# Optimization experiments

Measured on AMD Instinct MI355X. Metric: run time of the kernel, lower is better.

## Reference

```python
import jax, jax.numpy as jnp
import numpy as np

EPS = 1e-6
D_MODEL, D_HEAD, COND_F = 1024, 64, 768
N_HEADS = D_MODEL // D_HEAD
BATCH, SEQ = 2, 2048


def _rope_freqs(d_head, n_heads):
    # RoPE.__init__: dim = d_head // 2; count = n_heads * dim // 4 = n_heads * d_head // 8
    d8 = d_head // 8
    log_min, log_max = np.log(np.pi), np.log(10.0 * np.pi)
    f = np.exp(np.linspace(log_min, log_max, n_heads * d8 + 1, dtype=np.float64)[:-1])
    return jnp.asarray(f.reshape(d8, n_heads).T, dtype=jnp.float32)  # [nh, d8]


def _apply_rotary(x, theta):
    # x: [n, nh, l, e], theta: [n, nh, l, d8]; rotate first 2*d8 channels
    d = theta.shape[-1]
    x1, x2, rest = x[..., :d], x[..., d:2 * d], x[..., 2 * d:]
    cos, sin = jnp.cos(theta), jnp.sin(theta)
    y1 = x1 * cos - x2 * sin
    y2 = x2 * cos + x1 * sin
    return jnp.concatenate([y1, y2, rest], axis=-1)


def setup_inputs() -> dict:
    key = jax.random.key(0)
    ks = jax.random.split(key, 6)
    x = jax.random.normal(ks[0], (BATCH, SEQ, D_MODEL), dtype=jnp.float32)
    pos = jnp.broadcast_to(jnp.arange(SEQ, dtype=jnp.float32), (BATCH, SEQ))[..., None]
    cond = jax.random.normal(ks[1], (BATCH, COND_F), dtype=jnp.float32)
    w_norm = jax.random.normal(ks[2], (D_MODEL, COND_F), dtype=jnp.float32) * 0.02
    w_qkv = jax.random.normal(ks[3], (3 * D_MODEL, D_MODEL), dtype=jnp.float32) * 0.02
    scale = jnp.full((N_HEADS,), 10.0, dtype=jnp.float32)
    w_out = jax.random.normal(ks[4], (D_MODEL, D_MODEL), dtype=jnp.float32) * 0.02
    return {"x": x, "pos": pos, "cond": cond, "w_norm": w_norm,
            "w_qkv": w_qkv, "scale": scale, "w_out": w_out}


def reference(x, pos, cond, w_norm, w_qkv, scale, w_out):
    n, l, d = x.shape
    nh, e = N_HEADS, D_HEAD
    skip = x
    # AdaRMSNorm: scale = (linear(cond) + 1) * rsqrt(mean(x^2))
    cond_scale = cond @ w_norm.T + 1.0                      # [n, d]
    mean_sq = jnp.mean(x * x, axis=-1, keepdims=True)       # [n, l, 1]
    xn = x * (cond_scale[:, None, :] * jax.lax.rsqrt(mean_sq + EPS))
    # QKV projection
    qkv = (xn @ w_qkv.T).reshape(n, l, 3, nh, e)
    q = jnp.transpose(qkv[:, :, 0], (0, 2, 1, 3))           # [n, nh, l, e]
    k = jnp.transpose(qkv[:, :, 1], (0, 2, 1, 3))
    v = jnp.transpose(qkv[:, :, 2], (0, 2, 1, 3))
    # cosine-sim scaling
    sqrt_scale = jnp.sqrt(scale)[None, :, None, None]       # [1, nh, 1, 1]
    q = q * (sqrt_scale * jax.lax.rsqrt(jnp.sum(q * q, axis=-1, keepdims=True) + EPS))
    k = k * (sqrt_scale * jax.lax.rsqrt(jnp.sum(k * k, axis=-1, keepdims=True) + EPS))
    # RoPE: theta = pos[..., None] * freqs -> [n, l, nh, d8] -> [n, nh, l, d8]
    freqs = _rope_freqs(e, nh)
    theta = jnp.transpose(pos[..., None] * freqs, (0, 2, 1, 3))
    q = _apply_rotary(q, theta)
    k = _apply_rotary(k, theta)
    # attention with softmax scale = 1.0
    scores = jnp.einsum('nhle,nhme->nhlm', q, k)
    attn = jax.nn.softmax(scores, axis=-1)
    out = jnp.einsum('nhlm,nhme->nhle', attn, v)
    out = jnp.transpose(out, (0, 2, 1, 3)).reshape(n, l, d)
    return out @ w_out.T + skip
```

## Files before the change

kernel.cpp:

```cpp
#include <hip/hip_runtime.h>
#include <math.h>

#define D_MODEL 1024
#define D_HEAD  64
#define N_HEADS 16
#define COND_F  768
#define BATCH   2
#define SEQ     2048
#define NTOK    (BATCH*SEQ)
#define QKV_N   (3*D_MODEL)

typedef unsigned short u16;
typedef __attribute__((ext_vector_type(4))) float  f32x4;
typedef __attribute__((ext_vector_type(8))) __bf16 bfrag;
typedef __attribute__((ext_vector_type(4))) unsigned short u16x4;
typedef __attribute__((ext_vector_type(8))) unsigned short u16x8;

__device__ __forceinline__ u16 f2bf(float f) {
    unsigned u = __builtin_bit_cast(unsigned, f);
    return (u16)((u + 0x7fffu + ((u >> 16) & 1u)) >> 16);
}
__device__ __forceinline__ float bf2f(u16 h) {
    unsigned u = ((unsigned)h) << 16;
    return __builtin_bit_cast(float, u);
}

__device__ __forceinline__ float fexp2(float x) {
    float y;
    asm("v_exp_f32 %0, %1" : "=v"(y) : "v"(x));
    return y;
}

__device__ __forceinline__ void async16(const void* g, void* l) {
    __builtin_amdgcn_global_load_lds(
        (const __attribute__((address_space(1))) unsigned int*)g,
        (__attribute__((address_space(3))) unsigned int*)l, 16, 0, 0);
}

__global__ __launch_bounds__(256) void prep_kernel(const float* __restrict__ wqkv,
                                                   const float* __restrict__ wout,
                                                   u16* __restrict__ wqkv_b,
                                                   u16* __restrict__ wout_b,
                                                   const float* __restrict__ cond,
                                                   const float* __restrict__ w_norm,
                                                   float* __restrict__ cs,
                                                   const float* __restrict__ pos,
                                                   float2* __restrict__ tab) {
    if (blockIdx.x < 2048) {
        int i = blockIdx.x * 256 + threadIdx.x;
        const int n1 = QKV_N * D_MODEL / 8;
        const float* src; u16* dst; int off;
        if (i < n1) { src = wqkv; dst = wqkv_b; off = i * 8; }
        else        { src = wout; dst = wout_b; off = (i - n1) * 8; }
        float4 a = *(const float4*)(src + off);
        float4 b = *(const float4*)(src + off + 4);
        *(u16x4*)(dst + off)     = (u16x4){f2bf(a.x), f2bf(a.y), f2bf(a.z), f2bf(a.w)};
        *(u16x4*)(dst + off + 4) = (u16x4){f2bf(b.x), f2bf(b.y), f2bf(b.z), f2bf(b.w)};
    } else if (blockIdx.x < 2560) {
        int lane = threadIdx.x & 63, w = threadIdx.x >> 6;
        int wid = (blockIdx.x - 2048) * 4 + w;
        int b = wid >> 10, d = wid & 1023;
        const float* c = cond + b * COND_F;
        const float* wn = w_norm + (size_t)d * COND_F;
        float acc = 0.f;
        #pragma unroll
        for (int kk = 0; kk < 3; ++kk) {
            int j = kk * 256 + lane * 4;
            float4 cv = *(const float4*)(c + j);
            float4 wv = *(const float4*)(wn + j);
            acc += cv.x * wv.x + cv.y * wv.y + cv.z * wv.z + cv.w * wv.w;
        }
        for (int m = 1; m < 64; m <<= 1) acc += __shfl_xor(acc, m);
        if (lane == 0) cs[wid] = acc + 1.0f;
    } else {
        int i = (blockIdx.x - 2560) * 256 + threadIdx.x;
        int j = i & 7, h = (i >> 3) & 15;
        int s = (i >> 7) & 2047, b = i >> 18;
        double lf = 1.1447298858494001741 + (double)(j * 16 + h) * (2.302585092994045684 / 128.0);
        float fr = (float)exp(lf);
        float th = pos[b * SEQ + s] * fr;
        tab[i] = make_float2(cosf(th), sinf(th));
    }
}

__global__ __launch_bounds__(256) void rmsnorm_kernel(const float* __restrict__ x,
                                                      const float* __restrict__ cs,
                                                      u16* __restrict__ xn) {
    int tok = blockIdx.x, t = threadIdx.x;
    int b = tok >> 11;
    const float* xr = x + (size_t)tok * D_MODEL;
    float4 v = *(const float4*)(xr + t * 4);
    float ss = v.x * v.x + v.y * v.y + v.z * v.z + v.w * v.w;
    for (int m = 1; m < 64; m <<= 1) ss += __shfl_xor(ss, m);
    __shared__ float red[4];
    int w = t >> 6;
    if ((t & 63) == 0) red[w] = ss;
    __syncthreads();
    float tot = red[0] + red[1] + red[2] + red[3];
    float r = rsqrtf(tot * (1.0f / D_MODEL) + 1e-6f);
    float4 cv = *(const float4*)(cs + b * D_MODEL + t * 4);
    *(u16x4*)(xn + (size_t)tok * D_MODEL + t * 4) =
        (u16x4){f2bf(v.x * cv.x * r), f2bf(v.y * cv.y * r),
                f2bf(v.z * cv.z * r), f2bf(v.w * cv.w * r)};
}

template<int MODE>
__global__ __launch_bounds__(512) void gemm_bt(const u16* __restrict__ A, const u16* __restrict__ B,
                                               u16* __restrict__ Cq, u16* __restrict__ Ck,
                                               u16* __restrict__ Cv, float* __restrict__ Cf,
                                               const float* __restrict__ skip,
                                               const float* __restrict__ scale,
                                               const float2* __restrict__ tab,
                                               int M, int N, int K) {
    __shared__ u16 As[128 * 32];
    __shared__ u16 Bs[128 * 32];
    int tid = threadIdx.x;
    int lane = tid & 63, w = tid >> 6;
    int wr = w >> 1, wc = w & 1;
    int m0 = blockIdx.x * 128, n0 = blockIdx.y * 128;
    f32x4 acc[2][4] = {};
    const u16* Ag = A + (size_t)m0 * K;
    const u16* Bg = B + (size_t)n0 * K;
    int lr = lane & 15, lq = lane >> 4;

    int srow = tid >> 2, scol = (tid & 3) * 8;
    for (int kt = 0; kt < K; kt += 32) {
        __syncthreads();
        async16(Ag + (size_t)srow * K + kt + scol, &As[tid * 8]);
        async16(Bg + (size_t)srow * K + kt + scol, &Bs[tid * 8]);
        __syncthreads();
        bfrag af[2], bfv[4];
        #pragma unroll
        for (int fm = 0; fm < 2; ++fm)
            af[fm] = *(const bfrag*)&As[(wr * 32 + fm * 16 + lr) * 32 + lq * 8];
        #pragma unroll
        for (int fn = 0; fn < 4; ++fn)
            bfv[fn] = *(const bfrag*)&Bs[(wc * 64 + fn * 16 + lr) * 32 + lq * 8];
        #pragma unroll
        for (int fm = 0; fm < 2; ++fm)
            #pragma unroll
            for (int fn = 0; fn < 4; ++fn)
                acc[fm][fn] = __builtin_amdgcn_mfma_f32_16x16x32_bf16(af[fm], bfv[fn], acc[fm][fn], 0, 0, 0);
    }

    if (MODE == 1) {
        #pragma unroll
        for (int fm = 0; fm < 2; ++fm) {
            int rowbase = m0 + wr * 32 + fm * 16 + lq * 4;
            #pragma unroll
            for (int fn = 0; fn < 4; ++fn) {
                int col = n0 + wc * 64 + fn * 16 + lr;
                #pragma unroll
                for (int r = 0; r < 4; ++r) {
                    int row = rowbase + r;
                    Cf[(size_t)row * N + col] = acc[fm][fn][r] + skip[(size_t)row * N + col];
                }
            }
        }
    } else {
        int colbase0 = n0 + wc * 64;
        int sel = colbase0 >> 10;
        int h = (colbase0 >> 6) & 15;
        int bb = m0 >> 11;
        if (sel == 2) {
            #pragma unroll
            for (int fm = 0; fm < 2; ++fm) {
                int sP = (m0 & 2047) + wr * 32 + 8 * lq + 4 * fm;
                #pragma unroll
                for (int fn = 0; fn < 4; ++fn) {
                    int e = fn * 16 + lr;
                    u16x4 pk = {f2bf(acc[fm][fn][0]), f2bf(acc[fm][fn][1]),
                                f2bf(acc[fm][fn][2]), f2bf(acc[fm][fn][3])};
                    *(u16x4*)&Cv[((size_t)(bb * N_HEADS + h) * D_HEAD + e) * SEQ + sP] = pk;
                }
            }
        } else {
            u16* p = sel ? Ck : Cq;
            float sq = sqrtf(scale[h]);
            float mult = (sel == 0) ? sq * 1.4426950408889634f : sq;
            #pragma unroll
            for (int fm = 0; fm < 2; ++fm) {
                int s0 = (m0 & 2047) + wr * 32 + fm * 16 + lq * 4;
                #pragma unroll
                for (int r = 0; r < 4; ++r) {
                    float v0 = acc[fm][0][r], v1 = acc[fm][1][r],
                          v2 = acc[fm][2][r], v3 = acc[fm][3][r];
                    float ss = v0 * v0 + v1 * v1 + v2 * v2 + v3 * v3;
                    ss += __shfl_xor(ss, 1); ss += __shfl_xor(ss, 2);
                    ss += __shfl_xor(ss, 4); ss += __shfl_xor(ss, 8);
                    float rs = mult * rsqrtf(ss + 1e-6f);
                    v0 *= rs; v1 *= rs; v2 *= rs; v3 *= rs;
                    float part = __shfl_xor(v0, 8);
                    float2 cs2 = tab[(((size_t)bb * SEQ + (s0 + r)) * 16 + h) * 8 + (lr & 7)];
                    v0 = (lr < 8) ? v0 * cs2.x - part * cs2.y
                                  : v0 * cs2.x + part * cs2.y;
                    size_t rp = ((size_t)(bb * N_HEADS + h) * SEQ + (s0 + r)) * D_HEAD;
                    p[rp + lr]      = f2bf(v0);
                    p[rp + 16 + lr] = f2bf(v1);
                    p[rp + 32 + lr] = f2bf(v2);
                    p[rp + 48 + lr] = f2bf(v3);
                }
            }
        }
    }
}

__global__ __launch_bounds__(512) void attn_kernel(const u16* __restrict__ q,
                                                   const u16* __restrict__ k,
                                                   const u16* __restrict__ vt,
                                                   u16* __restrict__ o_part,
                                                   float* __restrict__ lsum_part) {
    __shared__ u16 Ks0[64 * 64];
    __shared__ u16 Ks1[64 * 64];
    __shared__ u16 Vs0[64 * 64];
    __shared__ u16 Vs1[64 * 64];
    int tid = threadIdx.x, lane = tid & 63, w = tid >> 6;
    int bh = blockIdx.y;
    int qs = blockIdx.x * 256;
    int z = blockIdx.z, nz = gridDim.z;
    int chunk = SEQ / nz;
    int kv0 = z * chunk;
    int lr = lane & 15, lq = lane >> 4;

    bfrag qf[2][2];
    #pragma unroll
    for (int mf = 0; mf < 2; ++mf) {
        const u16* qb = q + ((size_t)bh * SEQ + qs + w * 32 + mf * 16 + lr) * D_HEAD + lq * 8;
        qf[mf][0] = *(const bfrag*)qb;
        qf[mf][1] = *(const bfrag*)(qb + 32);
    }
    bfrag ones;
    #pragma unroll
    for (int j = 0; j < 8; ++j) ones[j] = (__bf16)1.0f;

    f32x4 oacc[2][4] = {};
    f32x4 oacc5[2] = {};
    const u16* kbase = k + (size_t)bh * SEQ * D_HEAD;
    const u16* vbase = vt + (size_t)bh * D_HEAD * SEQ;

    int srow = tid >> 3, scol = (tid & 7) ^ ((tid >> 3) & 7);
    const u16* kg = kbase + (size_t)srow * 64 + scol * 8;
    const u16* vg = vbase + (size_t)srow * SEQ + scol * 8;

    #define STAGE(kt, Kd, Vd) do { \
        async16(kg + (size_t)(kt) * 64, Kd + tid * 8); \
        async16(vg + (kt),              Vd + tid * 8); } while (0)

    auto tile_compute = [&](const u16* Kb, const u16* Vb) {
        f32x4 sacc[2][4] = {};
        __builtin_amdgcn_s_setprio(1);
        #pragma unroll
        for (int nb = 0; nb < 4; ++nb) {
            int row = nb * 16 + lr;
            #pragma unroll
            for (int kb = 0; kb < 2; ++kb) {
                bfrag kf = *(const bfrag*)&Kb[row * 64 + (((kb * 4 + lq) ^ (row & 7)) * 8)];
                sacc[0][nb] = __builtin_amdgcn_mfma_f32_16x16x32_bf16(kf, qf[0][kb], sacc[0][nb], 0, 0, 0);
                sacc[1][nb] = __builtin_amdgcn_mfma_f32_16x16x32_bf16(kf, qf[1][kb], sacc[1][nb], 0, 0, 0);
            }
        }
        __builtin_amdgcn_s_setprio(0);

        #pragma unroll
        for (int kb = 0; kb < 2; ++kb) {
            bfrag pf[2];
            #pragma unroll
            for (int mf = 0; mf < 2; ++mf)
                #pragma unroll
                for (int half = 0; half < 2; ++half) {
                    int nb = kb * 2 + half;
                    #pragma unroll
                    for (int r = 0; r < 4; ++r)
                        pf[mf][half * 4 + r] = (__bf16)fexp2(sacc[mf][nb][r]);
                }
            __builtin_amdgcn_s_setprio(1);
            oacc5[0] = __builtin_amdgcn_mfma_f32_16x16x32_bf16(pf[0], ones, oacc5[0], 0, 0, 0);
            oacc5[1] = __builtin_amdgcn_mfma_f32_16x16x32_bf16(pf[1], ones, oacc5[1], 0, 0, 0);
            #pragma unroll
            for (int eb = 0; eb < 4; ++eb) {
                int row = eb * 16 + lr;
                bfrag vf = *(const bfrag*)&Vb[row * 64 + (((kb * 4 + lq) ^ (row & 7)) * 8)];
                oacc[0][eb] = __builtin_amdgcn_mfma_f32_16x16x32_bf16(pf[0], vf, oacc[0][eb], 0, 0, 0);
                oacc[1][eb] = __builtin_amdgcn_mfma_f32_16x16x32_bf16(pf[1], vf, oacc[1][eb], 0, 0, 0);
            }
            __builtin_amdgcn_s_setprio(0);
        }
    };

    STAGE(kv0, Ks0, Vs0);
    __syncthreads();

    const int NTILE = chunk / 64;
    for (int t = 0; t < NTILE; t += 2) {
        if (t + 1 < NTILE) STAGE(kv0 + (t + 1) * 64, Ks1, Vs1);
        tile_compute(Ks0, Vs0);
        __syncthreads();
        if (t + 2 < NTILE) STAGE(kv0 + (t + 2) * 64, Ks0, Vs0);
        if (t + 1 < NTILE) {
            tile_compute(Ks1, Vs1);
            __syncthreads();
        }
    }
    #undef STAGE

    int b = bh >> 4, h = bh & 15;
    u16* op = o_part + (size_t)z * NTOK * D_MODEL;
    #pragma unroll
    for (int mf = 0; mf < 2; ++mf) {
        #pragma unroll
        for (int r = 0; r < 4; ++r) {
            int qrow = qs + w * 32 + mf * 16 + lq * 4 + r;
            if (lr == 0)
                lsum_part[((size_t)z * BATCH * N_HEADS + bh) * SEQ + qrow] = oacc5[mf][r];
            #pragma unroll
            for (int eb = 0; eb < 4; ++eb) {
                int e = eb * 16 + lr;
                op[((size_t)b * SEQ + qrow) * D_MODEL + h * D_HEAD + e] = f2bf(oacc[mf][eb][r]);
            }
        }
    }
}

__global__ __launch_bounds__(256) void combine_kernel(const u16* __restrict__ o_part,
                                                      const float* __restrict__ lsum_part,
                                                      u16* __restrict__ out, int Z) {
    int i = blockIdx.x * 256 + threadIdx.x;
    int base = i * 8;
    int t = base >> 10, col = base & 1023;
    int b = t >> 11, s = t & 2047, h = col >> 6;
    size_t li = (size_t)(b * N_HEADS + h) * SEQ + s;
    float lsum = 0.f;
    for (int z = 0; z < Z; ++z) lsum += lsum_part[(size_t)z * BATCH * N_HEADS * SEQ + li];
    float inv = 1.0f / lsum;
    float acc[8] = {};
    for (int z = 0; z < Z; ++z) {
        u16x8 a = *(const u16x8*)(o_part + (size_t)z * NTOK * D_MODEL + base);
        #pragma unroll
        for (int j = 0; j < 8; ++j) acc[j] += bf2f(a[j]);
    }
    u16x8 r;
    #pragma unroll
    for (int j = 0; j < 8; ++j) r[j] = f2bf(acc[j] * inv);
    *(u16x8*)(out + base) = r;
}

extern "C" void kernel_launch(void* const* d_in, const int* in_sizes, int n_in,
                              void* d_out, int out_size, void* d_ws, size_t ws_size,
                              hipStream_t stream) {
    const float* x      = (const float*)d_in[0];
    const float* pos    = (const float*)d_in[1];
    const float* cond   = (const float*)d_in[2];
    const float* w_norm = (const float*)d_in[3];
    const float* w_qkv  = (const float*)d_in[4];
    const float* scale  = (const float*)d_in[5];
    const float* w_out  = (const float*)d_in[6];
    float* out = (float*)d_out;

    char* ws = (char*)d_ws;
    u16* xn     = (u16*)ws;
    u16* wqkv_b = (u16*)(ws + (8u  << 20));
    u16* wout_b = (u16*)(ws + (14u << 20));
    float* cs   = (float*)(ws + (16u << 20));
    u16* qb     = (u16*)(ws + (16u << 20) + (1u << 16));
    const size_t HSZ = (size_t)BATCH * N_HEADS * SEQ * D_HEAD;
    u16* kb = qb + HSZ;
    u16* vt = kb + HSZ;
    u16* o_part   = (u16*)(ws + (41u << 20));
    float2* tab   = (float2*)(ws + (41u << 20));
    u16* attn_o = xn;

    size_t need4 = (41ull << 20) + 4 * ((size_t)NTOK * D_MODEL * 2) + 4 * ((size_t)BATCH * N_HEADS * SEQ * 4);
    int Z = (ws_size >= need4) ? 4 : 2;
    float* lsum_p = (float*)(ws + (41u << 20) + (size_t)Z * NTOK * D_MODEL * 2);

    prep_kernel<<<dim3(4608), dim3(256), 0, stream>>>(w_qkv, w_out, wqkv_b, wout_b,
                                                      cond, w_norm, cs, pos, (float2*)tab);
    rmsnorm_kernel<<<dim3(NTOK), dim3(256), 0, stream>>>(x, cs, xn);
    gemm_bt<0><<<dim3(NTOK / 128, QKV_N / 128), dim3(512), 0, stream>>>(
        xn, wqkv_b, qb, kb, vt, (float*)nullptr, (const float*)nullptr,
        scale, (const float2*)tab, NTOK, QKV_N, D_MODEL);
    attn_kernel<<<dim3(SEQ / 256, BATCH * N_HEADS, Z), dim3(512), 0, stream>>>(
        qb, kb, vt, o_part, lsum_p);
    combine_kernel<<<dim3(NTOK * D_MODEL / 8 / 256), dim3(256), 0, stream>>>(o_part, lsum_p, attn_o, Z);
    gemm_bt<1><<<dim3(NTOK / 128, D_MODEL / 128), dim3(512), 0, stream>>>(
        attn_o, wout_b, nullptr, nullptr, nullptr, out, x,
        (const float*)nullptr, (const float2*)nullptr, NTOK, D_MODEL, D_MODEL);
}
```

Measured before the change: 125.3 us.

## Double-buffer GEMM LDS loads and deepen attention KV prefetch with vmcnt waits

The bf16 GEMM now keeps two LDS buffers per operand and issues the async global-to-LDS loads for the next K-slice while the current one is being multiplied. It replaces the pair of __syncthreads per iteration with explicit s_waitcnt vmcnt counts plus scheduling barriers. The attention kernel now prefetches two K/V tiles ahead using the same wait scheme, so load latency can overlap with MFMA work. The risk is that the hard-coded vmcnt(2) assumes each stage issues exactly two loads per thread. If the attention STAGE issues more than that, tiles could be read before they have fully arrived.

After: 122.2 us. -2.4%, faster.

```diff
diff --git a/kernel.cpp b/kernel.cpp
--- a/kernel.cpp
+++ b/kernel.cpp
@@ -36,6 +36,12 @@
         (const __attribute__((address_space(1))) unsigned int*)g,
         (__attribute__((address_space(3))) unsigned int*)l, 16, 0, 0);
 }
+
+#define SBAR do { __builtin_amdgcn_sched_barrier(0); \
+                  __builtin_amdgcn_s_barrier(); \
+                  __builtin_amdgcn_sched_barrier(0); } while (0)
+#define WAITV2 do { asm volatile("s_waitcnt vmcnt(2)" ::: "memory"); } while (0)
+#define WAITV0 do { asm volatile("s_waitcnt vmcnt(0)" ::: "memory"); } while (0)
 
 __global__ __launch_bounds__(256) void prep_kernel(const float* __restrict__ wqkv,
                                                    const float* __restrict__ wout,
@@ -112,8 +118,10 @@
                                                const float* __restrict__ scale,
                                                const float2* __restrict__ tab,
                                                int M, int N, int K) {
-    __shared__ u16 As[128 * 32];
-    __shared__ u16 Bs[128 * 32];
+    __shared__ u16 As0[128 * 32];
+    __shared__ u16 As1[128 * 32];
+    __shared__ u16 Bs0[128 * 32];
+    __shared__ u16 Bs1[128 * 32];
     int tid = threadIdx.x;
     int lane = tid & 63, w = tid >> 6;
     int wr = w >> 1, wc = w & 1;
@@ -124,24 +132,45 @@
     int lr = lane & 15, lq = lane >> 4;
 
     int srow = tid >> 2, scol = (tid & 3) * 8;
-    for (int kt = 0; kt < K; kt += 32) {
-        __syncthreads();
-        async16(Ag + (size_t)srow * K + kt + scol, &As[tid * 8]);
-        async16(Bg + (size_t)srow * K + kt + scol, &Bs[tid * 8]);
-        __syncthreads();
+
+    #define GSTAGE(kt, Ad, Bd) do { \
+        async16(Ag + (size_t)srow * K + (kt) + scol, Ad + tid * 8); \
+        async16(Bg + (size_t)srow * K + (kt) + scol, Bd + tid * 8); } while (0)
+
+    auto compute = [&](const u16* Asb, const u16* Bsb) {
         bfrag af[2], bfv[4];
         #pragma unroll
         for (int fm = 0; fm < 2; ++fm)
-            af[fm] = *(const bfrag*)&As[(wr * 32 + fm * 16 + lr) * 32 + lq * 8];
+            af[fm] = *(const bfrag*)&Asb[(wr * 32 + fm * 16 + lr) * 32 + lq * 8];
         #pragma unroll
         for (int fn = 0; fn < 4; ++fn)
-            bfv[fn] = *(const bfrag*)&Bs[(wc * 64 + fn * 16 + lr) * 32 + lq * 8];
+            bfv[fn] = *(const bfrag*)&Bsb[(wc * 64 + fn * 16 + lr) * 32 + lq * 8];
         #pragma unroll
         for (int fm = 0; fm < 2; ++fm)
             #pragma unroll
             for (int fn = 0; fn < 4; ++fn)
                 acc[fm][fn] = __builtin_amdgcn_mfma_f32_16x16x32_bf16(af[fm], bfv[fn], acc[fm][fn], 0, 0, 0);
-    }
+    };
+
+    const int NK = K / 32;
+    GSTAGE(0, As0, Bs0);
+    GSTAGE(32, As1, Bs1);
+
+    for (int t = 0; t < NK; t += 2) {
+        if (t + 1 < NK) WAITV2; else WAITV0;
+        SBAR;
+        compute(As0, Bs0);
+        SBAR;
+        if (t + 2 < NK) GSTAGE((t + 2) * 32, As0, Bs0);
+        if (t + 1 < NK) {
+            if (t + 2 < NK) WAITV2; else WAITV0;
+            SBAR;
+            compute(As1, Bs1);
+            SBAR;
+            if (t + 3 < NK) GSTAGE((t + 3) * 32, As1, Bs1);
+        }
+    }
+    #undef GSTAGE
 
     if (MODE == 1) {
         #pragma unroll
@@ -287,18 +316,22 @@
         }
     };
 
+    const int NTILE = chunk / 64;
     STAGE(kv0, Ks0, Vs0);
-    __syncthreads();
-
-    const int NTILE = chunk / 64;
+    STAGE(kv0 + 64, Ks1, Vs1);
+
     for (int t = 0; t < NTILE; t += 2) {
-        if (t + 1 < NTILE) STAGE(kv0 + (t + 1) * 64, Ks1, Vs1);
+        if (t + 1 < NTILE) WAITV2; else WAITV0;
+        SBAR;
         tile_compute(Ks0, Vs0);
-        __syncthreads();
+        SBAR;
         if (t + 2 < NTILE) STAGE(kv0 + (t + 2) * 64, Ks0, Vs0);
         if (t + 1 < NTILE) {
+            if (t + 2 < NTILE) WAITV2; else WAITV0;
+            SBAR;
             tile_compute(Ks1, Vs1);
-            __syncthreads();
+            SBAR;
+            if (t + 3 < NTILE) STAGE(kv0 + (t + 3) * 64, Ks1, Vs1);
         }
     }
     #undef STAGE
```
